# Kernel tuning notes

Measured on AMD Instinct MI355X. Metric: run time of the kernel, lower is better.

Reference implementation:

```python
import math
import jax, jax.numpy as jnp
import numpy as np

B, L, D, K = 4, 8192, 256, 2
J = math.ceil(math.log((L - 1) / (K - 1) + 1) / math.log(K))  # 13


def setup_inputs() -> dict:
    key = jax.random.key(0)
    ks = jax.random.split(key, 6)
    h_scale = math.sqrt((math.gamma(K / 2) / math.gamma(J + K / 2)) ** (1.0 / J) / 2)
    return {
        "x": jax.random.normal(ks[0], (B, L, D), dtype=jnp.float32),
        "rms_scale": jnp.ones((D,), dtype=jnp.float32),
        "h0": h_scale * jax.random.normal(ks[1], (D, K), dtype=jnp.float32),
        "h1": h_scale * jax.random.normal(ks[2], (D, K), dtype=jnp.float32),
        "w": (1.0 / math.sqrt(J + 2)) * jax.random.normal(ks[3], (J + 2, D), dtype=jnp.float32),
        "conv_w": jax.random.normal(ks[4], (D, 2 * D), dtype=jnp.float32) / math.sqrt(D),
        "conv_b": jnp.zeros((2 * D,), dtype=jnp.float32),
    }


def _dw_conv(a, h, dilation, d):
    # depthwise dilated 1D conv, VALID padding; a: [B, Lpad, D], h: [1, D, K]
    return jax.lax.conv_general_dilated(
        lhs=a, rhs=h, window_strides=(1,), padding='VALID',
        dimension_numbers=('NLC', 'IOL', 'NLC'),
        rhs_dilation=(dilation,), feature_group_count=d)


def reference(x, rms_scale, h0, h1, w, conv_w, conv_b):
    d = x.shape[-1]
    k = h0.shape[-1]
    n_levels = w.shape[0] - 2
    skip = x
    # RMSNorm (flax default eps=1e-6)
    x = x * jax.lax.rsqrt(jnp.mean(jnp.square(x), axis=-1, keepdims=True) + 1e-6) * rms_scale
    # MultiResLayer (pad_right=False -> left pad, causal)
    h0e = h0[None, :, :]  # [1, D, K]
    h1e = h1[None, :, :]
    y = jnp.zeros_like(x)
    a = x
    for j in range(n_levels):
        dilation = k ** j
        pad = dilation * (k - 1)
        a = jnp.pad(a, ((0, 0), (pad, 0), (0, 0)))
        b = _dw_conv(a, h1e, dilation, d)
        a = _dw_conv(a, h0e, dilation, d)
        y = y + w[j + 1][None, None, :] * b
    y = y + w[None, :1, :] * x + w[None, -1:, :] * a
    # activation -> pointwise conv to 2D -> GLU -> residual
    y = jax.nn.gelu(y)  # approximate=True matches flax nn.gelu default
    y = jnp.einsum('bld,de->ble', y, conv_w) + conv_b
    y = jax.nn.glu(y, axis=-1)
    return y + skip
```

## Files before the change

kernel.cpp:

```cpp
#include <hip/hip_runtime.h>
#include <hip/hip_bf16.h>

#define B_ 4
#define L_ 8192
#define D_ 256
#define J_ 13

typedef __attribute__((ext_vector_type(4))) float f32x4;
typedef __attribute__((ext_vector_type(2))) float v2f;
typedef __attribute__((ext_vector_type(8))) short bf16x8;
typedef __attribute__((ext_vector_type(8))) unsigned short u16x8;

__device__ __forceinline__ void async_copy16(const void* g, void* l) {
    __builtin_amdgcn_global_load_lds(
        (const __attribute__((address_space(1))) void*)g,
        (__attribute__((address_space(3))) void*)l, 16, 0, 0);
}

__device__ __forceinline__ unsigned int cvtpk(float lo, float hi) {
    unsigned int r;
    asm("v_cvt_pk_bf16_f32 %0, %1, %2" : "=v"(r) : "v"(lo), "v"(hi));
    return r;
}
__device__ __forceinline__ unsigned short packbf1(float a) {
    return (unsigned short)((__float_as_uint(a) + 0x8000u) >> 16);
}
__device__ __forceinline__ float bflo(unsigned int u) { return __uint_as_float(u << 16); }
__device__ __forceinline__ float bfhi(unsigned int u) { return __uint_as_float(u & 0xFFFF0000u); }

__global__ void rms_wt_kernel(const float* __restrict__ x, const float* __restrict__ scale,
                              ushort* __restrict__ xtb,
                              const float* __restrict__ W, ushort* __restrict__ Wt) {
    __shared__ __align__(16) float sm[32 * 260 + 32];
    int blk = blockIdx.x;
    int tid = threadIdx.x;
    if (blk < 32) {
        float (*tile)[65] = (float(*)[65])sm;
        int dt = blk >> 3, et = blk & 7;
        int d0 = dt * 64, e0 = et * 64;
#pragma unroll
        for (int k = 0; k < 16; ++k) {
            int i = tid + k * 256;
            int r = i >> 6, c = i & 63;
            tile[r][c] = W[(d0 + r) * 512 + e0 + c];
        }
        __syncthreads();
#pragma unroll
        for (int k = 0; k < 16; ++k) {
            int i = tid + k * 256;
            int r = i >> 6, c = i & 63;
            Wt[(e0 + r) * 256 + d0 + c] = packbf1(tile[c][r]);
        }
        return;
    }
    blk -= 32;
    float (*tile)[260] = (float(*)[260])sm;
    float* invl = sm + 32 * 260;
    int b  = blk >> 8;
    int l0 = (blk & 255) << 5;
    const float* src = x + ((size_t)(b * L_ + l0)) * D_;
#pragma unroll
    for (int k = 0; k < 8; ++k) {
        int i = tid + k * 256;
        int r = i >> 6, c4 = i & 63;
        *(float4*)&tile[r][c4 * 4] = *(const float4*)(src + r * D_ + c4 * 4);
    }
    __syncthreads();
    int wave = tid >> 6, lane = tid & 63;
#pragma unroll
    for (int rr = 0; rr < 8; ++rr) {
        int r = wave * 8 + rr;
        float s = 0.f;
#pragma unroll
        for (int q = 0; q < 4; ++q) { float v = tile[r][lane + 64 * q]; s += v * v; }
#pragma unroll
        for (int off = 32; off; off >>= 1) s += __shfl_xor(s, off);
        if (lane == 0) invl[r] = rsqrtf(s * (1.0f / 256.0f) + 1e-6f);
    }
    __syncthreads();
    uint* dst32 = (uint*)xtb;
#pragma unroll
    for (int k = 0; k < 16; ++k) {
        int i = tid + k * 256;
        int d = i >> 4, lp = (i & 15) * 2;
        float v0 = tile[lp][d]     * invl[lp]     * scale[d];
        float v1 = tile[lp + 1][d] * invl[lp + 1] * scale[d];
        dst32[(((size_t)(b * D_ + d)) * L_ + l0 + lp) >> 1] = cvtpk(v0, v1);
    }
}

#define LEVEL_SMALL(d, jj, buf)                                                  \
    do {                                                                         \
        uint4 pk;                                                                \
        pk.x = cvtpk(cc[8][0],  cc[8][1]);  pk.y = cvtpk(cc[9][0],  cc[9][1]);   \
        pk.z = cvtpk(cc[10][0], cc[10][1]); pk.w = cvtpk(cc[11][0], cc[11][1]);  \
        *(uint4*)((buf) + slot + 16) = pk;                                       \
        pk.x = cvtpk(cc[12][0], cc[12][1]); pk.y = cvtpk(cc[13][0], cc[13][1]);  \
        pk.z = cvtpk(cc[14][0], cc[14][1]); pk.w = cvtpk(cc[15][0], cc[15][1]);  \
        *(uint4*)((buf) + slot + 24) = pk;                                       \
        __syncthreads();                                                         \
        v2f pt2[8];                                                              \
        if (ct > 0) {                                                            \
            uint4 a  = *(const uint4*)((buf) + slot - 40 + 16);                  \
            uint4 bq = *(const uint4*)((buf) + slot - 40 + 24);                  \
            uint uu[8] = {a.x, a.y, a.z, a.w, bq.x, bq.y, bq.z, bq.w};           \
            _Pragma("unroll") for (int q = 0; q < 8; ++q) {                      \
                pt2[q][0] = bflo(uu[q]); pt2[q][1] = bfhi(uu[q]); }              \
        } else { _Pragma("unroll") for (int q = 0; q < 8; ++q) pt2[q] = (v2f)0.f; } \
        float wjs = w[((jj) + 1) * D_ + c];                                      \
        v2f wh10 = (v2f)(wjs * h10), wh11 = (v2f)(wjs * h11);                    \
        v2f h00v = (v2f)h00, h01v = (v2f)h01;                                    \
        _Pragma("unroll")                                                        \
        for (int p = 15; p >= 0; --p) {                                          \
            v2f pv;                                                              \
            if ((d) == 1) {                                                      \
                pv[0] = (p == 0) ? pt2[7][1] : cc[p - 1][1];                     \
                pv[1] = cc[p][0];                                                \
            } else {                                                             \
                const int hd = (d) >> 1;                                         \
                pv = (p >= hd) ? cc[p - hd] : pt2[8 + p - hd];                   \
            }                                                                    \
            v2f nv = h00v * pv + h01v * cc[p];                                   \
            y[p] += wh10 * pv;                                                   \
            y[p] += wh11 * cc[p];                                                \
            cc[p] = nv;                                                          \
        }                                                                        \
    } while (0)

__global__ void __launch_bounds__(256) cascade_kernel(
    const ushort* __restrict__ xt, const float* __restrict__ h0,
    const float* __restrict__ h1, const float* __restrict__ w,
    ushort* __restrict__ ygt) {
    __shared__ __align__(16) ushort ex[2 * 256 * 40];
    ushort* bufA = ex;
    ushort* bufB = ex + 256 * 40;
    int blk = blockIdx.x;
    int b = blk >> 8;
    int c = blk & 255;
    int ct = threadIdx.x;
    int slot = ct * 40;
    float h00 = h0[2*c], h01 = h0[2*c+1];
    float h10 = h1[2*c], h11 = h1[2*c+1];
    float w0 = w[c], wlast = w[14 * D_ + c];

    const ushort* src = xt + ((size_t)(b * D_ + c)) * L_ + ct * 32;
    v2f cc[16], y[16];
#pragma unroll
    for (int m = 0; m < 4; ++m) {
        u16x8 v = *(const u16x8*)(src + m * 8);
#pragma unroll
        for (int p = 0; p < 4; ++p) {
            cc[m*4+p][0] = __uint_as_float(((uint)v[2*p])     << 16);
            cc[m*4+p][1] = __uint_as_float(((uint)v[2*p + 1]) << 16);
        }
    }
    {
        v2f w0v = (v2f)w0;
#pragma unroll
        for (int p = 0; p < 16; ++p) y[p] = w0v * cc[p];
    }

    LEVEL_SMALL(1, 0, bufA);
    LEVEL_SMALL(2, 1, bufB);
    LEVEL_SMALL(4, 2, bufA);
    LEVEL_SMALL(8, 3, bufB);
    LEVEL_SMALL(16, 4, bufA);

#pragma unroll 1
    for (int j = 5; j < J_; ++j) {
        int dT = 1 << (j - 5);
        float wjs = w[(j + 1) * D_ + c];
        v2f wh10 = (v2f)(wjs * h10), wh11 = (v2f)(wjs * h11);
        v2f h00v = (v2f)h00, h01v = (v2f)h01;
        ushort* buf = (j & 1) ? bufB : bufA;
#pragma unroll
        for (int m = 0; m < 4; ++m) {
            uint4 pk;
            pk.x = cvtpk(cc[4*m][0],   cc[4*m][1]);
            pk.y = cvtpk(cc[4*m+1][0], cc[4*m+1][1]);
            pk.z = cvtpk(cc[4*m+2][0], cc[4*m+2][1]);
            pk.w = cvtpk(cc[4*m+3][0], cc[4*m+3][1]);
            *(uint4*)(buf + slot + 8 * m) = pk;
        }
        __syncthreads();
        bool has = (ct >= dT);
        int pbase = slot - dT * 40;
        v2f pv2[16];
        if (has) {
#pragma unroll
            for (int m = 0; m < 4; ++m) {
                uint4 a = *(const uint4*)(buf + pbase + 8 * m);
                uint uu[4] = {a.x, a.y, a.z, a.w};
#pragma unroll
                for (int q = 0; q < 4; ++q) {
                    pv2[4*m+q][0] = bflo(uu[q]);
                    pv2[4*m+q][1] = bfhi(uu[q]);
                }
            }
        } else {
#pragma unroll
            for (int q = 0; q < 16; ++q) pv2[q] = (v2f)0.f;
        }
#pragma unroll
        for (int p = 0; p < 16; ++p) {
            v2f nv = h00v * pv2[p] + h01v * cc[p];
            y[p] += wh10 * pv2[p];
            y[p] += wh11 * cc[p];
            cc[p] = nv;
        }
    }
    ushort* dst = ygt + ((size_t)(b * D_ + c)) * L_ + ct * 32;
    v2f wl2 = (v2f)wlast;
    v2f c1v = (v2f)0.044715f, onev = (v2f)1.f;
    v2f k2v = (v2f)-2.3022083f;
#pragma unroll
    for (int m = 0; m < 4; ++m) {
        uint pk4[4];
#pragma unroll
        for (int q = 0; q < 4; ++q) {
            int p = 4*m + q;
            v2f v  = y[p] + wl2 * cc[p];
            v2f vv = v * v;
            v2f tt = c1v * vv + onev;
            v2f q2 = k2v * (v * tt);
            float g0 = v[0] * __builtin_amdgcn_rcpf(1.f + exp2f(q2[0]));
            float g1 = v[1] * __builtin_amdgcn_rcpf(1.f + exp2f(q2[1]));
            pk4[q] = cvtpk(g0, g1);
        }
        uint4 pk; pk.x = pk4[0]; pk.y = pk4[1]; pk.z = pk4[2]; pk.w = pk4[3];
        *(uint4*)(dst + 8 * m) = pk;
    }
}

__global__ void __launch_bounds__(256) gemm_kernel(
    const ushort* __restrict__ ygt, const ushort* __restrict__ Wt,
    const float* __restrict__ cb, const float* __restrict__ x,
    float* __restrict__ out) {
    __shared__ __align__(16) char smem[32768];
    ushort* As = (ushort*)smem;
    ushort* Bs = As + 128 * 64;
    int hw = blockIdx.x;
    int blk = (hw & 7) * 128 + (hw >> 3);
    int b = blk >> 8;
    int rem = blk & 255;
    int ltile = rem >> 2, et = rem & 3;
    int l0 = ltile * 128, e0 = et * 64;
    int tid = threadIdx.x;
    int wave = tid >> 6, lane = tid & 63;
    int wm = wave >> 1, wn = wave & 1;
    int m0 = wm * 64;

    int srow_in = (lane >> 3);
    int sg = lane & 7;
    int sgg = sg ^ srow_in;

    int lb = tid & 15, db = tid >> 4;
    const ushort* aPtr = ygt + ((size_t)(b * D_ + db * 4)) * L_ + l0 + lb * 8;

    f32x4 acc[4][4];
#pragma unroll
    for (int i = 0; i < 4; ++i)
#pragma unroll
        for (int j = 0; j < 4; ++j) acc[i][j] = (f32x4)0.f;

    uint4 ar[4];
#pragma unroll
    for (int rr = 0; rr < 4; ++rr) ar[rr] = *(const uint4*)(aPtr + rr * L_);

#pragma unroll
    for (int kc = 0; kc < 4; ++kc) {
        __syncthreads();
#pragma unroll
        for (int v = 0; v < 4; ++v) {
            int r = wave * 32 + v * 8 + srow_in;
            int e = (r < 64) ? (e0 + r) : (256 + e0 + (r - 64));
            async_copy16(Wt + e * 256 + kc * 64 + sgg * 8,
                         Bs + r * 64 + sg * 8);
        }
        __builtin_amdgcn_sched_barrier(0);
#pragma unroll
        for (int j = 0; j < 8; ++j) {
            int q = j >> 1;
            uint sel = (j & 1) ? 0x07060302u : 0x05040100u;
            uint w0 = __builtin_amdgcn_perm(((const uint*)&ar[1])[q],
                                            ((const uint*)&ar[0])[q], sel);
            uint w1 = __builtin_amdgcn_perm(((const uint*)&ar[3])[q],
                                            ((const uint*)&ar[2])[q], sel);
            uint2 wv; wv.x = w0; wv.y = w1;
            int r = lb * 8 + j;
            *(uint2*)(As + r * 64 + (((db >> 1) ^ j ^ (lb & 7)) * 8) + (db & 1) * 4) = wv;
        }
        if (kc < 3) {
#pragma unroll
            for (int rr = 0; rr < 4; ++rr)
                ar[rr] = *(const uint4*)(aPtr + (size_t)(kc + 1) * 64 * L_ + rr * L_);
            __builtin_amdgcn_sched_barrier(0);
            asm volatile("s_waitcnt vmcnt(4) lgkmcnt(0)" ::: "memory");
        } else {
            __builtin_amdgcn_sched_barrier(0);
            asm volatile("s_waitcnt vmcnt(0) lgkmcnt(0)" ::: "memory");
        }
        __builtin_amdgcn_s_barrier();
        __builtin_amdgcn_sched_barrier(0);
#pragma unroll
        for (int kk = 0; kk < 2; ++kk) {
            bf16x8 af[4], bfr[4];
            int g = kk * 4 + (lane >> 4);
            int gp = (g ^ (lane & 7)) * 8;
#pragma unroll
            for (int mt = 0; mt < 4; ++mt) {
                int rowA = m0 + mt * 16 + (lane & 15);
                int gpA = (g ^ (lane & 7) ^ ((rowA >> 3) & 7)) * 8;
                af[mt] = *(const bf16x8*)(As + rowA * 64 + gpA);
            }
#pragma unroll
            for (int nt = 0; nt < 4; ++nt) {
                int n = wn * 32 + (nt & 1) * 16 + (nt >> 1) * 64 + (lane & 15);
                bfr[nt] = *(const bf16x8*)(Bs + n * 64 + gp);
            }
#pragma unroll
            for (int mt = 0; mt < 4; ++mt)
#pragma unroll
                for (int nt = 0; nt < 4; ++nt)
                    acc[mt][nt] = __builtin_amdgcn_mfma_f32_16x16x32_bf16(
                        af[mt], bfr[nt], acc[mt][nt], 0, 0, 0);
        }
    }
    __syncthreads();
    float* epi = (float*)smem;
    int row_in = (lane >> 4) * 4;
    int col = lane & 15;
#pragma unroll
    for (int mt = 0; mt < 4; ++mt) {
#pragma unroll
        for (int p = 0; p < 2; ++p) {
            f32x4 uacc = acc[mt][p];
            f32x4 vacc = acc[mt][p + 2];
            int ee = wn * 32 + p * 16 + col;
            float bu = cb[e0 + ee], bv = cb[256 + e0 + ee];
#pragma unroll
            for (int r = 0; r < 4; ++r) {
                int ll = m0 + mt * 16 + row_in + r;
                float u = uacc[r] + bu;
                float v = vacc[r] + bv;
                float g = u * __builtin_amdgcn_rcpf(1.f + __expf(-v));
                epi[ll * 64 + (ee ^ ((ll & 4) ? 16 : 0))] = g;
            }
        }
    }
    __syncthreads();
#pragma unroll
    for (int k = 0; k < 8; ++k) {
        int i = tid + k * 256;
        int ll = i >> 4, e4 = i & 15;
        int exo = (e4 * 4) ^ ((ll & 4) ? 16 : 0);
        float4 gv = *(const float4*)(epi + ll * 64 + exo);
        size_t gidx = ((size_t)(b * L_ + l0 + ll)) * D_ + e0 + e4 * 4;
        float4 xv = *(const float4*)(x + gidx);
        float4 ov;
        ov.x = gv.x + xv.x; ov.y = gv.y + xv.y;
        ov.z = gv.z + xv.z; ov.w = gv.w + xv.w;
        *(float4*)(out + gidx) = ov;
    }
}

extern "C" void kernel_launch(void* const* d_in, const int* in_sizes, int n_in,
                              void* d_out, int out_size, void* d_ws, size_t ws_size,
                              hipStream_t stream) {
    const float* x  = (const float*)d_in[0];
    const float* rs = (const float*)d_in[1];
    const float* h0 = (const float*)d_in[2];
    const float* h1 = (const float*)d_in[3];
    const float* w  = (const float*)d_in[4];
    const float* cw = (const float*)d_in[5];
    const float* cb = (const float*)d_in[6];
    float* out = (float*)d_out;
    char* ws = (char*)d_ws;

    ushort* xtb = (ushort*)ws;
    ushort* ygt = (ushort*)(ws + 16777216);
    ushort* Wt  = (ushort*)(ws + 33554432);

    rms_wt_kernel<<<1056, 256, 0, stream>>>(x, rs, xtb, cw, Wt);
    cascade_kernel<<<1024, 256, 0, stream>>>(xtb, h0, h1, w, ygt);
    gemm_kernel<<<1024, 256, 0, stream>>>(ygt, Wt, cb, x, out);
}
```

Baseline: 142.8 us.

## Use halo recomputation for small levels and transposed layout for large-dilation levels

The first five cascade levels no longer exchange data through LDS with barriers. Each thread instead loads the previous thread's 32-element chunk from global memory as a halo and recomputes its cascade redundantly. Levels 5-7 keep the LDS exchange. Levels 8-12 transpose the state in LDS so each thread holds strided elements, which makes dilations 256-4096 register-local shifts and avoids a barrier per level. This trades extra halo FLOPs, extra global loads and register pressure (cch, cs, ys arrays) for fewer __syncthreads and LDS round trips, and adds another bf16 rounding of the partial y.

Result: slower. 153.4 us (+7.5%).

```diff
diff --git a/kernel.cpp b/kernel.cpp
--- a/kernel.cpp
+++ b/kernel.cpp
@@ -89,41 +89,92 @@
     }
 }
 
-#define LEVEL_SMALL(d, jj, buf)                                                  \
+#define HLEVEL(dd, jj)                                                           \
     do {                                                                         \
-        uint4 pk;                                                                \
-        pk.x = cvtpk(cc[8][0],  cc[8][1]);  pk.y = cvtpk(cc[9][0],  cc[9][1]);   \
-        pk.z = cvtpk(cc[10][0], cc[10][1]); pk.w = cvtpk(cc[11][0], cc[11][1]);  \
-        *(uint4*)((buf) + slot + 16) = pk;                                       \
-        pk.x = cvtpk(cc[12][0], cc[12][1]); pk.y = cvtpk(cc[13][0], cc[13][1]);  \
-        pk.z = cvtpk(cc[14][0], cc[14][1]); pk.w = cvtpk(cc[15][0], cc[15][1]);  \
-        *(uint4*)((buf) + slot + 24) = pk;                                       \
+        float wjs = w[((jj) + 1) * D_ + c];                                      \
+        v2f wh10 = (v2f)(wjs * h10), wh11 = (v2f)(wjs * h11);                    \
+        v2f h00v = (v2f)h00, h01v = (v2f)h01;                                    \
+        const int hd = (dd) >> 1;                                                \
+        _Pragma("unroll")                                                        \
+        for (int p = 15; p >= 0; --p) {           \
+            v2f pv;                                                              \
+            if ((dd) == 1) {                                                     \
+                pv[0] = (p == 0) ? cch[15][1] : cc[p - 1][1];                    \
+                pv[1] = cc[p][0];                                                \
+            } else {                                                             \
+                pv = (p >= hd) ? cc[p - hd] : cch[16 - hd + p];                  \
+            }                                                                    \
+            v2f nv = h00v * pv + h01v * cc[p];                                   \
+            y[p] += wh10 * pv;                                                   \
+            y[p] += wh11 * cc[p];                                                \
+            cc[p] = nv;                                                          \
+        }                                                                        \
+        _Pragma("unroll")                                                        \
+        for (int p = 15; p >= 0; --p) {          \
+            v2f pvh;                                                             \
+            if ((dd) == 1) {                                                     \
+                pvh[0] = (p == 0) ? 0.f : cch[p - 1][1];                         \
+                pvh[1] = cch[p][0];                                              \
+            } else {                                                             \
+                pvh = (p >= hd) ? cch[p - hd] : (v2f)0.f;                        \
+            }                                                                    \
+            cch[p] = h00v * pvh + h01v * cch[p];                                 \
+        }                                                                        \
+    } while (0)
+
+#define BIGLEVEL(dT, jj, buf)                                                    \
+    do {                                                                         \
+        float wjs = w[((jj) + 1) * D_ + c];                                      \
+        v2f wh10 = (v2f)(wjs * h10), wh11 = (v2f)(wjs * h11);                    \
+        v2f h00v = (v2f)h00, h01v = (v2f)h01;                                    \
+        _Pragma("unroll")                                                        \
+        for (int m = 0; m < 4; ++m) {                                            \
+            uint4 pk;                                                            \
+            pk.x = cvtpk(cc[4*m][0],   cc[4*m][1]);                              \
+            pk.y = cvtpk(cc[4*m+1][0], cc[4*m+1][1]);                            \
+            pk.z = cvtpk(cc[4*m+2][0], cc[4*m+2][1]);                            \
+            pk.w = cvtpk(cc[4*m+3][0], cc[4*m+3][1]);                            \
+            *(uint4*)((buf) + slot + 8 * m) = pk;                                \
+        }                                                                        \
         __syncthreads();                                                         \
-        v2f pt2[8];                                                              \
-        if (ct > 0) {                                                            \
-            uint4 a  = *(const uint4*)((buf) + slot - 40 + 16);                  \
-            uint4 bq = *(const uint4*)((buf) + slot - 40 + 24);                  \
-            uint uu[8] = {a.x, a.y, a.z, a.w, bq.x, bq.y, bq.z, bq.w};           \
-            _Pragma("unroll") for (int q = 0; q < 8; ++q) {                      \
-                pt2[q][0] = bflo(uu[q]); pt2[q][1] = bfhi(uu[q]); }              \
-        } else { _Pragma("unroll") for (int q = 0; q < 8; ++q) pt2[q] = (v2f)0.f; } \
+        bool has = (ct >= (dT));                                                 \
+        int pbase = slot - (dT) * 40;                                            \
+        v2f pv2[16];                                                             \
+        if (has) {                                                               \
+            _Pragma("unroll")                                                    \
+            for (int m = 0; m < 4; ++m) {                                        \
+                uint4 a = *(const uint4*)((buf) + pbase + 8 * m);                \
+                uint uu[4] = {a.x, a.y, a.z, a.w};                               \
+                _Pragma("unroll")                                                \
+                for (int q = 0; q < 4; ++q) {                                    \
+                    pv2[4*m+q][0] = bflo(uu[q]);                                 \
+                    pv2[4*m+q][1] = bfhi(uu[q]);                                 \
+                }                                                                \
+            }                                                                    \
+        } else {                                                                 \
+            _Pragma("unroll") for (int q = 0; q < 16; ++q) pv2[q] = (v2f)0.f;    \
+        }                                                                        \
+        _Pragma("unroll")                                                        \
+        for (int p = 0; p < 16; ++p) {                                           \
+            v2f nv = h00v * pv2[p] + h01v * cc[p];                               \
+            y[p] += wh10 * pv2[p];                                               \
+            y[p] += wh11 * cc[p];                                                \
+            cc[p] = nv;                                                          \
+        }                                                                        \
+    } while (0)
+
+#define TAILLEVEL(dm, jj)                                                        \
+    do {                                                                         \
         float wjs = w[((jj) + 1) * D_ + c];                                      \
         v2f wh10 = (v2f)(wjs * h10), wh11 = (v2f)(wjs * h11);                    \
         v2f h00v = (v2f)h00, h01v = (v2f)h01;                                    \
         _Pragma("unroll")                                                        \
         for (int p = 15; p >= 0; --p) {                                          \
-            v2f pv;                                                              \
-            if ((d) == 1) {                                                      \
-                pv[0] = (p == 0) ? pt2[7][1] : cc[p - 1][1];                     \
-                pv[1] = cc[p][0];                                                \
-            } else {                                                             \
-                const int hd = (d) >> 1;                                         \
-                pv = (p >= hd) ? cc[p - hd] : pt2[8 + p - hd];                   \
-            }                                                                    \
-            v2f nv = h00v * pv + h01v * cc[p];                                   \
-            y[p] += wh10 * pv;                                                   \
-            y[p] += wh11 * cc[p];                                                \
-            cc[p] = nv;                                                          \
+            v2f pv = (p >= (dm)) ? cs[p - (dm)] : (v2f)0.f;                      \
+            v2f nv = h00v * pv + h01v * cs[p];                                   \
+            ys[p] += wh10 * pv;                                                  \
+            ys[p] += wh11 * cs[p];                                               \
+            cs[p] = nv;                                                          \
         }                                                                        \
     } while (0)
 
@@ -132,8 +183,10 @@
     const float* __restrict__ h1, const float* __restrict__ w,
     ushort* __restrict__ ygt) {
     __shared__ __align__(16) ushort ex[2 * 256 * 40];
-    ushort* bufA = ex;
-    ushort* bufB = ex + 256 * 40;
+    ushort* EXA = ex;
+    ushort* EXB = ex + 256 * 40;
+    uint* FLA = (uint*)EXA;
+    uint* FLB = (uint*)EXB;
     int blk = blockIdx.x;
     int b = blk >> 8;
     int c = blk & 255;
@@ -143,36 +196,48 @@
     float h10 = h1[2*c], h11 = h1[2*c+1];
     float w0 = w[c], wlast = w[14 * D_ + c];
 
-    const ushort* src = xt + ((size_t)(b * D_ + c)) * L_ + ct * 32;
-    v2f cc[16], y[16];
+    const ushort* srow = xt + ((size_t)(b * D_ + c)) * L_;
+    v2f cc[16], cch[16], y[16];
 #pragma unroll
     for (int m = 0; m < 4; ++m) {
-        u16x8 v = *(const u16x8*)(src + m * 8);
+        u16x8 v = *(const u16x8*)(srow + ct * 32 + m * 8);
 #pragma unroll
         for (int p = 0; p < 4; ++p) {
             cc[m*4+p][0] = __uint_as_float(((uint)v[2*p])     << 16);
             cc[m*4+p][1] = __uint_as_float(((uint)v[2*p + 1]) << 16);
         }
     }
+    if (ct > 0) {
+#pragma unroll
+        for (int m = 0; m < 4; ++m) {
+            u16x8 v = *(const u16x8*)(srow + (ct - 1) * 32 + m * 8);
+#pragma unroll
+            for (int p = 0; p < 4; ++p) {
+                cch[m*4+p][0] = __uint_as_float(((uint)v[2*p])     << 16);
+                cch[m*4+p][1] = __uint_as_float(((uint)v[2*p + 1]) << 16);
+            }
+        }
+    } else {
+#pragma unroll
+        for (int p = 0; p < 16; ++p) cch[p] = (v2f)0.f;
+    }
     {
         v2f w0v = (v2f)w0;
 #pragma unroll
         for (int p = 0; p < 16; ++p) y[p] = w0v * cc[p];
     }
 
-    LEVEL_SMALL(1, 0, bufA);
-    LEVEL_SMALL(2, 1, bufB);
-    LEVEL_SMALL(4, 2, bufA);
-    LEVEL_SMALL(8, 3, bufB);
-    LEVEL_SMALL(16, 4, bufA);
-
-#pragma unroll 1
-    for (int j = 5; j < J_; ++j) {
-        int dT = 1 << (j - 5);
-        float wjs = w[(j + 1) * D_ + c];
-        v2f wh10 = (v2f)(wjs * h10), wh11 = (v2f)(wjs * h11);
-        v2f h00v = (v2f)h00, h01v = (v2f)h01;
-        ushort* buf = (j & 1) ? bufB : bufA;
+    HLEVEL(1, 0);
+    HLEVEL(2, 1);
+    HLEVEL(4, 2);
+    HLEVEL(8, 3);
+    HLEVEL(16, 4);
+
+    BIGLEVEL(1, 5, EXB);
+    BIGLEVEL(2, 6, EXA);
+    BIGLEVEL(4, 7, EXB);
+
+    {
 #pragma unroll
         for (int m = 0; m < 4; ++m) {
             uint4 pk;
@@ -180,35 +245,76 @@
             pk.y = cvtpk(cc[4*m+1][0], cc[4*m+1][1]);
             pk.z = cvtpk(cc[4*m+2][0], cc[4*m+2][1]);
             pk.w = cvtpk(cc[4*m+3][0], cc[4*m+3][1]);
-            *(uint4*)(buf + slot + 8 * m) = pk;
-        }
+            *((uint4*)(FLA + 16 * ct) + m) = pk;
+        }
+    }
+    __syncthreads();
+    v2f cs[16], ys[16];
+#pragma unroll
+    for (int m = 0; m < 16; ++m) {
+        uint u = FLA[ct + 256 * m];
+        cs[m][0] = bflo(u); cs[m][1] = bfhi(u);
+        ys[m] = (v2f)0.f;
+    }
+
+    {
+        float wjs = w[9 * D_ + c];
+        v2f wh10 = (v2f)(wjs * h10), wh11 = (v2f)(wjs * h11);
+        v2f h00v = (v2f)h00, h01v = (v2f)h01;
+#pragma unroll
+        for (int m = 0; m < 16; ++m) FLB[ct + 256 * m] = cvtpk(cs[m][0], cs[m][1]);
         __syncthreads();
-        bool has = (ct >= dT);
-        int pbase = slot - dT * 40;
-        v2f pv2[16];
-        if (has) {
-#pragma unroll
-            for (int m = 0; m < 4; ++m) {
-                uint4 a = *(const uint4*)(buf + pbase + 8 * m);
-                uint uu[4] = {a.x, a.y, a.z, a.w};
-#pragma unroll
-                for (int q = 0; q < 4; ++q) {
-                    pv2[4*m+q][0] = bflo(uu[q]);
-                    pv2[4*m+q][1] = bfhi(uu[q]);
-                }
+#pragma unroll
+        for (int p = 15; p >= 0; --p) {
+            v2f pv;
+            if (p == 0) {
+                if (ct >= 128) { uint u = FLB[ct - 128]; pv[0] = bflo(u); pv[1] = bfhi(u); }
+                else pv = (v2f)0.f;
+            } else {
+                uint u = FLB[ct + 256 * p - 128];
+                pv[0] = bflo(u); pv[1] = bfhi(u);
             }
-        } else {
-#pragma unroll
-            for (int q = 0; q < 16; ++q) pv2[q] = (v2f)0.f;
-        }
-#pragma unroll
-        for (int p = 0; p < 16; ++p) {
-            v2f nv = h00v * pv2[p] + h01v * cc[p];
-            y[p] += wh10 * pv2[p];
-            y[p] += wh11 * cc[p];
-            cc[p] = nv;
-        }
-    }
+            v2f nv = h00v * pv + h01v * cs[p];
+            ys[p] += wh10 * pv;
+            ys[p] += wh11 * cs[p];
+            cs[p] = nv;
+        }
+    }
+
+    TAILLEVEL(1, 9);
+    TAILLEVEL(2, 10);
+    TAILLEVEL(4, 11);
+    TAILLEVEL(8, 12);
+
+#pragma unroll
+    for (int m = 0; m < 16; ++m) FLA[ct + 256 * m] = cvtpk(cs[m][0], cs[m][1]);
+    __syncthreads();
+    v2f ctb[16];
+#pragma unroll
+    for (int m = 0; m < 4; ++m) {
+        uint4 a = *((const uint4*)(FLA + 16 * ct) + m);
+        uint uu[4] = {a.x, a.y, a.z, a.w};
+#pragma unroll
+        for (int q = 0; q < 4; ++q) {
+            ctb[4*m+q][0] = bflo(uu[q]);
+            ctb[4*m+q][1] = bfhi(uu[q]);
+        }
+    }
+#pragma unroll
+    for (int m = 0; m < 16; ++m) FLB[ct + 256 * m] = cvtpk(ys[m][0], ys[m][1]);
+    __syncthreads();
+    v2f ytb[16];
+#pragma unroll
+    for (int m = 0; m < 4; ++m) {
+        uint4 a = *((const uint4*)(FLB + 16 * ct) + m);
+        uint uu[4] = {a.x, a.y, a.z, a.w};
+#pragma unroll
+        for (int q = 0; q < 4; ++q) {
+            ytb[4*m+q][0] = bflo(uu[q]);
+            ytb[4*m+q][1] = bfhi(uu[q]);
+        }
+    }
+
     ushort* dst = ygt + ((size_t)(b * D_ + c)) * L_ + ct * 32;
     v2f wl2 = (v2f)wlast;
     v2f c1v = (v2f)0.044715f, onev = (v2f)1.f;
@@ -219,7 +325,7 @@
 #pragma unroll
         for (int q = 0; q < 4; ++q) {
             int p = 4*m + q;
-            v2f v  = y[p] + wl2 * cc[p];
+            v2f v  = (y[p] + ytb[p]) + wl2 * ctb[p];
             v2f vv = v * v;
             v2f tt = c1v * vv + onev;
             v2f q2 = k2v * (v * tt);
```

## Fuse cascade levels in pairs to halve LDS exchanges and barriers

Applied to the files above, without the earlier changes.

The dilated-conv cascade now processes two levels per shared-memory exchange. Each thread reads three shifted neighbour values and computes the intermediate level-j output in registers before applying level j+1. This cuts the number of __syncthreads and LDS round-trips from thirteen to seven. In exchange it adds extra LDS reads and FMAs for the recomputed intermediate, plus higher register pressure. Intermediate values also skip bf16 rounding, which slightly changes numerics.

Measured after the change: 348.3 us. 2.44x slower.

```diff
diff --git a/kernel.cpp b/kernel.cpp
--- a/kernel.cpp
+++ b/kernel.cpp
@@ -89,41 +89,71 @@
     }
 }
 
-#define LEVEL_SMALL(d, jj, buf)                                                  \
+#define UNP4(dst, has, off, buf)                                                 \
+    do {                                                                         \
+        if (has) {                                                               \
+            uint4 a_ = *(const uint4*)((buf) + (off));                           \
+            dst[0][0]=bflo(a_.x); dst[0][1]=bfhi(a_.x);                          \
+            dst[1][0]=bflo(a_.y); dst[1][1]=bfhi(a_.y);                          \
+            dst[2][0]=bflo(a_.z); dst[2][1]=bfhi(a_.z);                          \
+            dst[3][0]=bflo(a_.w); dst[3][1]=bfhi(a_.w);                          \
+        } else {                                                                 \
+            dst[0]=(v2f)0.f; dst[1]=(v2f)0.f; dst[2]=(v2f)0.f; dst[3]=(v2f)0.f; \
+        }                                                                        \
+    } while (0)
+
+#define PAIR_UPDATE(p, SA, S2, S3)                                               \
+    do {                                                                         \
+        v2f pvA = (SA);                                                          \
+        v2f pvB = h00v * (S3) + h01v * (S2);                                     \
+        v2f aj1 = h00v * pvA + h01v * cc[p];                                     \
+        y[p] += whA10 * pvA;  y[p] += whA11 * cc[p];                             \
+        y[p] += whB10 * pvB;  y[p] += whB11 * aj1;                               \
+        cc[p] = h00v * pvB + h01v * aj1;                                         \
+    } while (0)
+
+#define WTOP16(buf)                                                              \
     do {                                                                         \
         uint4 pk;                                                                \
-        pk.x = cvtpk(cc[8][0],  cc[8][1]);  pk.y = cvtpk(cc[9][0],  cc[9][1]);   \
-        pk.z = cvtpk(cc[10][0], cc[10][1]); pk.w = cvtpk(cc[11][0], cc[11][1]);  \
+        pk.x = cvtpk(cc[8][0],cc[8][1]);   pk.y = cvtpk(cc[9][0],cc[9][1]);      \
+        pk.z = cvtpk(cc[10][0],cc[10][1]); pk.w = cvtpk(cc[11][0],cc[11][1]);    \
         *(uint4*)((buf) + slot + 16) = pk;                                       \
-        pk.x = cvtpk(cc[12][0], cc[12][1]); pk.y = cvtpk(cc[13][0], cc[13][1]);  \
-        pk.z = cvtpk(cc[14][0], cc[14][1]); pk.w = cvtpk(cc[15][0], cc[15][1]);  \
+        pk.x = cvtpk(cc[12][0],cc[12][1]); pk.y = cvtpk(cc[13][0],cc[13][1]);    \
+        pk.z = cvtpk(cc[14][0],cc[14][1]); pk.w = cvtpk(cc[15][0],cc[15][1]);    \
         *(uint4*)((buf) + slot + 24) = pk;                                       \
+    } while (0)
+
+#define WFULL32(buf)                                                             \
+    do {                                                                         \
+        _Pragma("unroll")                                                        \
+        for (int m_ = 0; m_ < 4; ++m_) {                                         \
+            uint4 pk;                                                            \
+            pk.x = cvtpk(cc[4*m_][0],   cc[4*m_][1]);                            \
+            pk.y = cvtpk(cc[4*m_+1][0], cc[4*m_+1][1]);                          \
+            pk.z = cvtpk(cc[4*m_+2][0], cc[4*m_+2][1]);                          \
+            pk.w = cvtpk(cc[4*m_+3][0], cc[4*m_+3][1]);                          \
+            *(uint4*)((buf) + slot + 8 * m_) = pk;                               \
+        }                                                                        \
+    } while (0)
+
+#define BIGPAIR(dT, jA, buf)                                                     \
+    do {                                                                         \
+        float wA = w[((jA) + 1) * D_ + c], wB = w[((jA) + 2) * D_ + c];          \
+        v2f whA10 = (v2f)(wA * h10), whA11 = (v2f)(wA * h11);                    \
+        v2f whB10 = (v2f)(wB * h10), whB11 = (v2f)(wB * h11);                    \
+        v2f h00v = (v2f)h00, h01v = (v2f)h01;                                    \
+        WFULL32(buf);                                                            \
         __syncthreads();                                                         \
-        v2f pt2[8];                                                              \
-        if (ct > 0) {                                                            \
-            uint4 a  = *(const uint4*)((buf) + slot - 40 + 16);                  \
-            uint4 bq = *(const uint4*)((buf) + slot - 40 + 24);                  \
-            uint uu[8] = {a.x, a.y, a.z, a.w, bq.x, bq.y, bq.z, bq.w};           \
-            _Pragma("unroll") for (int q = 0; q < 8; ++q) {                      \
-                pt2[q][0] = bflo(uu[q]); pt2[q][1] = bfhi(uu[q]); }              \
-        } else { _Pragma("unroll") for (int q = 0; q < 8; ++q) pt2[q] = (v2f)0.f; } \
-        float wjs = w[((jj) + 1) * D_ + c];                                      \
-        v2f wh10 = (v2f)(wjs * h10), wh11 = (v2f)(wjs * h11);                    \
-        v2f h00v = (v2f)h00, h01v = (v2f)h01;                                    \
+        bool h1_ = (ct >= (dT)), h2_ = (ct >= 2*(dT)), h3_ = (ct >= 3*(dT));     \
+        int b1_ = slot - (dT)*40, b2_ = slot - 2*(dT)*40, b3_ = slot - 3*(dT)*40;\
         _Pragma("unroll")                                                        \
-        for (int p = 15; p >= 0; --p) {                                          \
-            v2f pv;                                                              \
-            if ((d) == 1) {                                                      \
-                pv[0] = (p == 0) ? pt2[7][1] : cc[p - 1][1];                     \
-                pv[1] = cc[p][0];                                                \
-            } else {                                                             \
-                const int hd = (d) >> 1;                                         \
-                pv = (p >= hd) ? cc[p - hd] : pt2[8 + p - hd];                   \
-            }                                                                    \
-            v2f nv = h00v * pv + h01v * cc[p];                                   \
-            y[p] += wh10 * pv;                                                   \
-            y[p] += wh11 * cc[p];                                                \
-            cc[p] = nv;                                                          \
+        for (int m = 0; m < 4; ++m) {                                            \
+            v2f s1[4], s2[4], s3[4];                                             \
+            UNP4(s1, h1_, b1_ + 8*m, buf);                                       \
+            UNP4(s2, h2_, b2_ + 8*m, buf);                                       \
+            UNP4(s3, h3_, b3_ + 8*m, buf);                                       \
+            _Pragma("unroll")                                                    \
+            for (int q = 0; q < 4; ++q) PAIR_UPDATE(4*m + q, s1[q], s2[q], s3[q]);\
         }                                                                        \
     } while (0)
 
@@ -160,55 +190,91 @@
         for (int p = 0; p < 16; ++p) y[p] = w0v * cc[p];
     }
 
-    LEVEL_SMALL(1, 0, bufA);
-    LEVEL_SMALL(2, 1, bufB);
-    LEVEL_SMALL(4, 2, bufA);
-    LEVEL_SMALL(8, 3, bufB);
-    LEVEL_SMALL(16, 4, bufA);
-
-#pragma unroll 1
-    for (int j = 5; j < J_; ++j) {
-        int dT = 1 << (j - 5);
-        float wjs = w[(j + 1) * D_ + c];
+    {
+        WTOP16(bufA);
+        __syncthreads();
+        v2f hp[2];
+        if (ct > 0) {
+            uint2 a2 = *(const uint2*)(bufA + slot - 40 + 28);
+            hp[0][0] = bflo(a2.x); hp[0][1] = bfhi(a2.x);
+            hp[1][0] = bflo(a2.y); hp[1][1] = bfhi(a2.y);
+        } else { hp[0] = (v2f)0.f; hp[1] = (v2f)0.f; }
+        float wjs = w[1 * D_ + c];
         v2f wh10 = (v2f)(wjs * h10), wh11 = (v2f)(wjs * h11);
         v2f h00v = (v2f)h00, h01v = (v2f)h01;
-        ushort* buf = (j & 1) ? bufB : bufA;
-#pragma unroll
-        for (int m = 0; m < 4; ++m) {
-            uint4 pk;
-            pk.x = cvtpk(cc[4*m][0],   cc[4*m][1]);
-            pk.y = cvtpk(cc[4*m+1][0], cc[4*m+1][1]);
-            pk.z = cvtpk(cc[4*m+2][0], cc[4*m+2][1]);
-            pk.w = cvtpk(cc[4*m+3][0], cc[4*m+3][1]);
-            *(uint4*)(buf + slot + 8 * m) = pk;
-        }
-        __syncthreads();
-        bool has = (ct >= dT);
-        int pbase = slot - dT * 40;
-        v2f pv2[16];
-        if (has) {
-#pragma unroll
-            for (int m = 0; m < 4; ++m) {
-                uint4 a = *(const uint4*)(buf + pbase + 8 * m);
-                uint uu[4] = {a.x, a.y, a.z, a.w};
-#pragma unroll
-                for (int q = 0; q < 4; ++q) {
-                    pv2[4*m+q][0] = bflo(uu[q]);
-                    pv2[4*m+q][1] = bfhi(uu[q]);
-                }
-            }
-        } else {
-#pragma unroll
-            for (int q = 0; q < 16; ++q) pv2[q] = (v2f)0.f;
-        }
-#pragma unroll
-        for (int p = 0; p < 16; ++p) {
-            v2f nv = h00v * pv2[p] + h01v * cc[p];
-            y[p] += wh10 * pv2[p];
+#pragma unroll
+        for (int p = 15; p >= 0; --p) {
+            v2f pv;
+            pv[0] = (p == 0) ? hp[1][1] : cc[p - 1][1];
+            pv[1] = cc[p][0];
+            v2f nv = h00v * pv + h01v * cc[p];
+            y[p] += wh10 * pv;
             y[p] += wh11 * cc[p];
             cc[p] = nv;
         }
     }
+
+    {
+        float wA = w[2 * D_ + c], wB = w[3 * D_ + c];
+        v2f whA10 = (v2f)(wA * h10), whA11 = (v2f)(wA * h11);
+        v2f whB10 = (v2f)(wB * h10), whB11 = (v2f)(wB * h11);
+        v2f h00v = (v2f)h00, h01v = (v2f)h01;
+        WTOP16(bufB);
+        __syncthreads();
+        v2f hp[8];
+        if (ct > 0) {
+            uint4 a  = *(const uint4*)(bufB + slot - 40 + 16);
+            uint4 bq = *(const uint4*)(bufB + slot - 40 + 24);
+            uint uu[8] = {a.x, a.y, a.z, a.w, bq.x, bq.y, bq.z, bq.w};
+#pragma unroll
+            for (int q = 0; q < 8; ++q) { hp[q][0] = bflo(uu[q]); hp[q][1] = bfhi(uu[q]); }
+        } else {
+#pragma unroll
+            for (int q = 0; q < 8; ++q) hp[q] = (v2f)0.f;
+        }
+#pragma unroll
+        for (int p = 15; p >= 0; --p) {
+            v2f S1 = (p >= 1) ? cc[p-1] : hp[7+p];
+            v2f S2 = (p >= 2) ? cc[p-2] : hp[6+p];
+            v2f S3 = (p >= 3) ? cc[p-3] : hp[5+p];
+            PAIR_UPDATE(p, S1, S2, S3);
+        }
+    }
+
+    {
+        float wA = w[4 * D_ + c], wB = w[5 * D_ + c];
+        v2f whA10 = (v2f)(wA * h10), whA11 = (v2f)(wA * h11);
+        v2f whB10 = (v2f)(wB * h10), whB11 = (v2f)(wB * h11);
+        v2f h00v = (v2f)h00, h01v = (v2f)h01;
+        WFULL32(bufA);
+        __syncthreads();
+        v2f hpF[12];
+        if (ct > 0) {
+            uint4 a0 = *(const uint4*)(bufA + slot - 40 + 8);
+            uint4 a1 = *(const uint4*)(bufA + slot - 40 + 16);
+            uint4 a2 = *(const uint4*)(bufA + slot - 40 + 24);
+            uint uu[12] = {a0.x, a0.y, a0.z, a0.w, a1.x, a1.y, a1.z, a1.w,
+                           a2.x, a2.y, a2.z, a2.w};
+#pragma unroll
+            for (int q = 0; q < 12; ++q) { hpF[q][0] = bflo(uu[q]); hpF[q][1] = bfhi(uu[q]); }
+        } else {
+#pragma unroll
+            for (int q = 0; q < 12; ++q) hpF[q] = (v2f)0.f;
+        }
+#pragma unroll
+        for (int p = 15; p >= 0; --p) {
+            v2f S4  = (p >= 4)  ? cc[p-4]  : hpF[8+p];
+            v2f S8  = (p >= 8)  ? cc[p-8]  : hpF[4+p];
+            v2f S12 = (p >= 12) ? cc[p-12] : hpF[p];
+            PAIR_UPDATE(p, S4, S8, S12);
+        }
+    }
+
+    BIGPAIR(1,  5, bufB);
+    BIGPAIR(4,  7, bufA);
+    BIGPAIR(16, 9, bufB);
+    BIGPAIR(64, 11, bufA);
+
     ushort* dst = ygt + ((size_t)(b * D_ + c)) * L_ + ct * 32;
     v2f wl2 = (v2f)wlast;
     v2f c1v = (v2f)0.044715f, onev = (v2f)1.f;
```
